# Performance work log

Hardware: AMD Instinct MI355X
Metric: run time of the kernel (lower is better)

Reference implementation:

```python
import jax, jax.numpy as jnp
import numpy as np

LN_EPS = 1e-5


def _layernorm_hd(x, gamma, beta):
    # normalize jointly over the last two dims (H, D), matching nn.LayerNorm((H, D))
    m = jnp.mean(x, axis=(-2, -1), keepdims=True)
    v = jnp.var(x, axis=(-2, -1), keepdims=True)
    return (x - m) * jax.lax.rsqrt(v + LN_EPS) * gamma + beta


def setup_inputs() -> dict:
    B, S, H, D = 4, 4096, 8, 64
    key = jax.random.key(0)
    k1, k2, k3 = jax.random.split(key, 3)
    heads_input = jax.random.normal(k1, (B, S, H, D), dtype=jnp.float32)
    W_hid = jax.random.normal(k2, (2 * D, 3 * D), dtype=jnp.float32) * (1.0 / np.sqrt(2 * D))
    b_hid = jnp.zeros((3 * D,), dtype=jnp.float32)
    W_og = jax.random.normal(k3, (2 * D, D), dtype=jnp.float32) * (1.0 / np.sqrt(2 * D))
    b_og = jnp.zeros((D,), dtype=jnp.float32)
    ln_gamma = jnp.ones((H, D), dtype=jnp.float32)
    ln_beta = jnp.zeros((H, D), dtype=jnp.float32)
    init_cx = jnp.zeros((H, D), dtype=jnp.float32)
    return {"heads_input": heads_input, "W_hid": W_hid, "b_hid": b_hid,
            "W_og": W_og, "b_og": b_og, "ln_gamma": ln_gamma,
            "ln_beta": ln_beta, "init_cx": init_cx}


def reference(heads_input, W_hid, b_hid, W_og, b_og, ln_gamma, ln_beta, init_cx):
    B, S, H, D = heads_input.shape
    # RS1cumsumFunc: exclusive (right-shifted) cumsum along seq of detached input
    x_det = jax.lax.stop_gradient(heads_input)
    cs = jnp.cumsum(x_det, axis=1)
    csum_raw = jnp.concatenate([jnp.zeros_like(cs[:, :1]), cs[:, :-1]], axis=1)
    csum = _layernorm_hd(csum_raw, ln_gamma, ln_beta)

    # trans_hid on concat(heads_input, csum): [B,S,H,2D] -> [B,S,H,3D]
    hid_in = jnp.concatenate([heads_input, csum], axis=-1)
    h3 = jnp.einsum('bshd,de->bshe', hid_in, W_hid) + b_hid
    igate, fgate, hidden = jnp.split(h3, 3, axis=-1)
    fg = jax.nn.sigmoid(fgate)
    igh = jax.nn.sigmoid(igate) * jax.nn.relu(hidden)

    # LGateFunc: cell_t = fg_t * cell_{t-1} + igh_t, cell_{-1} = init_cx
    def combine(c1, c2):
        a1, b1 = c1
        a2, b2 = c2
        return a1 * a2, b1 * a2 + b2

    a, b = jax.lax.associative_scan(combine, (fg, igh), axis=1)
    cell = a * init_cx + b  # init_cx [H,D] broadcasts over [B,S,H,D]

    og_in = jnp.concatenate([heads_input, cell], axis=-1)
    og = jax.nn.sigmoid(jnp.einsum('bshd,de->bshe', og_in, W_og) + b_og)
    return og * cell
```

## Files before the change

kernel.cpp:

```cpp
#include <hip/hip_runtime.h>
#include <math.h>

#define S_   4096
#define H_   8
#define D_   64
#define HD_  512
#define NCH  256
#define LCH  16
#define RC   128

typedef __bf16 bf16x8 __attribute__((ext_vector_type(8)));
typedef float  f32x4  __attribute__((ext_vector_type(4)));

__device__ __forceinline__ float sigm(float v) { return 1.f / (1.f + __expf(-v)); }

__global__ __launch_bounds__(256) void k_wt(const float* __restrict__ Wh,
                                            const float* __restrict__ Wo,
                                            __bf16* __restrict__ WthS,
                                            __bf16* __restrict__ WtoS) {
  int idx = blockIdx.x * 256 + threadIdx.x;
  if (idx < 24576) {
    int k = idx / 192, n = idx % 192;
    int nt = n >> 4, l16 = n & 15;
    int ks = k >> 5, quad = (k >> 3) & 3, j = k & 7;
    WthS[(((ks * 12 + nt) * 64) + quad * 16 + l16) * 8 + j] = (__bf16)Wh[idx];
  } else {
    int j2 = idx - 24576;
    int k = j2 >> 6, n = j2 & 63;
    int nt = n >> 4, l16 = n & 15;
    int ks = k >> 5, quad = (k >> 3) & 3, j = k & 7;
    WtoS[(((ks * 4 + nt) * 64) + quad * 16 + l16) * 8 + j] = (__bf16)Wo[j2];
  }
}

__global__ __launch_bounds__(512) void k_pre(const float* __restrict__ x,
                                             float* __restrict__ sums,
                                             __bf16* __restrict__ Abf) {
  const int t = threadIdx.x, h = t >> 6, d = t & 63;
  const int b = blockIdx.x >> 8, c = blockIdx.x & 255;
  const float* p = x + ((size_t)(b * S_ + c * LCH)) * HD_ + t;
  const size_t rT0 = ((size_t)(b * H_ + h)) * S_ + c * LCH;
  float acc = 0.f;
  #pragma unroll
  for (int i = 0; i < LCH; ++i) {
    float v = p[(size_t)i * HD_];
    acc += v;
    Abf[(rT0 + i) * 128 + d] = (__bf16)v;
  }
  sums[(size_t)blockIdx.x * HD_ + t] = acc;
}

__global__ __launch_bounds__(512) void k_scan_offsets(const float* __restrict__ sums,
                                                      float* __restrict__ offs) {
  const int b = blockIdx.x, t = threadIdx.x;
  float run = 0.f;
  #pragma unroll 16
  for (int c = 0; c < NCH; ++c) {
    size_t idx = ((size_t)b * NCH + c) * HD_ + t;
    float v = sums[idx];
    offs[idx] = run;
    run += v;
  }
}

__global__ __launch_bounds__(512) void k_ln(const float* __restrict__ offs,
                                            const float* __restrict__ gamma,
                                            const float* __restrict__ beta,
                                            __bf16* __restrict__ Abf) {
  __shared__ float2 red[2][8];
  const int t = threadIdx.x, h = t >> 6, d = t & 63;
  const int b = blockIdx.x >> 8, c = blockIdx.x & 255;
  const size_t rT0 = ((size_t)(b * H_ + h)) * S_ + c * LCH;
  float run = offs[(size_t)blockIdx.x * HD_ + t];
  const float g = gamma[t], be = beta[t];
  for (int i = 0; i < LCH; ++i) {
    float xv = (float)Abf[(rT0 + i) * 128 + d];
    float v = run, v2 = run * run;
    #pragma unroll
    for (int o = 32; o; o >>= 1) { v += __shfl_xor(v, o); v2 += __shfl_xor(v2, o); }
    if ((t & 63) == 0) red[i & 1][h] = make_float2(v, v2);
    __syncthreads();
    float s1 = 0.f, s2 = 0.f;
    #pragma unroll
    for (int w = 0; w < 8; ++w) { s1 += red[i & 1][w].x; s2 += red[i & 1][w].y; }
    float m = s1 * (1.f / HD_);
    float var = fmaf(-m, m, s2 * (1.f / HD_));
    float inv = rsqrtf(var + 1e-5f);
    Abf[(rT0 + i) * 128 + 64 + d] = (__bf16)((run - m) * inv * g + be);
    run += xv;
  }
}

__global__ __launch_bounds__(256) void k_gates(const __bf16* __restrict__ Abf,
                                               const __bf16* __restrict__ WthS,
                                               const float* __restrict__ bh,
                                               float* __restrict__ cA,
                                               float* __restrict__ cB) {
  const int t = threadIdx.x;
  const int wave = t >> 6, lane = t & 63;
  const int quad = lane >> 4, l16 = lane & 15;
  const int b = blockIdx.x >> 8, c = blockIdx.x & 255;

  f32x4 acc[2][12];
  #pragma unroll
  for (int i = 0; i < 2; ++i)
    #pragma unroll
    for (int j = 0; j < 12; ++j) acc[i][j] = (f32x4){0.f, 0.f, 0.f, 0.f};

  #pragma unroll
  for (int ks = 0; ks < 4; ++ks) {
    bf16x8 bfrag[12];
    #pragma unroll
    for (int nt = 0; nt < 12; ++nt)
      bfrag[nt] = *(const bf16x8*)(WthS + (size_t)((ks * 12 + nt) * 64 + lane) * 8);
    #pragma unroll
    for (int mi = 0; mi < 2; ++mi) {
      int h = wave * 2 + mi;
      size_t arow = ((size_t)(b * H_ + h)) * S_ + c * LCH + l16;
      bf16x8 afrag = *(const bf16x8*)(Abf + arow * 128 + ks * 32 + quad * 8);
      #pragma unroll
      for (int nt = 0; nt < 12; ++nt)
        acc[mi][nt] = __builtin_amdgcn_mfma_f32_16x16x32_bf16(afrag, bfrag[nt], acc[mi][nt], 0, 0, 0);
    }
  }

  #pragma unroll
  for (int mi = 0; mi < 2; ++mi) {
    int h = wave * 2 + mi;
    #pragma unroll
    for (int nt = 0; nt < 4; ++nt) {
      int d = nt * 16 + l16;
      float bi = bh[d], bf = bh[64 + d], bhv = bh[128 + d];
      float A = 1.f, Bv = 0.f;
      #pragma unroll
      for (int r = 0; r < 4; ++r) {
        float f = sigm(acc[mi][nt + 4][r] + bf);
        float g = sigm(acc[mi][nt][r] + bi) * fmaxf(acc[mi][nt + 8][r] + bhv, 0.f);
        A = f * A;
        Bv = fmaf(f, Bv, g);
      }
      float At = 0.f, Bt = 0.f;
      #pragma unroll
      for (int q = 0; q < 4; ++q) {
        float Aq = __shfl(A, q * 16 + l16);
        float Bq = __shfl(Bv, q * 16 + l16);
        if (q == 0) { At = Aq; Bt = Bq; }
        else { At = Aq * At; Bt = fmaf(Aq, Bt, Bq); }
      }
      if (quad == 0) {
        cA[(size_t)blockIdx.x * HD_ + h * 64 + d] = At;
        cB[(size_t)blockIdx.x * HD_ + h * 64 + d] = Bt;
      }
    }
  }
}

__global__ __launch_bounds__(512) void k_cell_scan(const float* __restrict__ cA,
                                                   const float* __restrict__ cB,
                                                   const float* __restrict__ initcx,
                                                   float* __restrict__ cin) {
  const int b = blockIdx.x, t = threadIdx.x;
  float run = initcx[t];
  #pragma unroll 16
  for (int c = 0; c < NCH; ++c) {
    size_t idx = ((size_t)b * NCH + c) * HD_ + t;
    float a = cA[idx], bb = cB[idx];
    cin[idx] = run;
    run = fmaf(a, run, bb);
  }
}

__global__ __launch_bounds__(256) void k_og(const __bf16* __restrict__ Abf,
                                            const __bf16* __restrict__ WthS,
                                            const float* __restrict__ bh,
                                            const __bf16* __restrict__ WtoS,
                                            const float* __restrict__ bo,
                                            const float* __restrict__ cin,
                                            float* __restrict__ out) {
  __shared__ float cl[RC * 68];
  const int t = threadIdx.x;
  const int wave = t >> 6, lane = t & 63;
  const int quad = lane >> 4, l16 = lane & 15;
  const int b = blockIdx.x >> 8, c = blockIdx.x & 255;

  f32x4 acc[2][12];
  #pragma unroll
  for (int i = 0; i < 2; ++i)
    #pragma unroll
    for (int j = 0; j < 12; ++j) acc[i][j] = (f32x4){0.f, 0.f, 0.f, 0.f};

  #pragma unroll
  for (int ks = 0; ks < 4; ++ks) {
    bf16x8 bfrag[12];
    #pragma unroll
    for (int nt = 0; nt < 12; ++nt)
      bfrag[nt] = *(const bf16x8*)(WthS + (size_t)((ks * 12 + nt) * 64 + lane) * 8);
    #pragma unroll
    for (int mi = 0; mi < 2; ++mi) {
      int h = wave * 2 + mi;
      size_t arow = ((size_t)(b * H_ + h)) * S_ + c * LCH + l16;
      bf16x8 afrag = *(const bf16x8*)(Abf + arow * 128 + ks * 32 + quad * 8);
      #pragma unroll
      for (int nt = 0; nt < 12; ++nt)
        acc[mi][nt] = __builtin_amdgcn_mfma_f32_16x16x32_bf16(afrag, bfrag[nt], acc[mi][nt], 0, 0, 0);
    }
  }

  #pragma unroll
  for (int mi = 0; mi < 2; ++mi) {
    int h = wave * 2 + mi;
    #pragma unroll
    for (int nt = 0; nt < 4; ++nt) {
      int d = nt * 16 + l16;
      float bi = bh[d], bf = bh[64 + d], bhv = bh[128 + d];
      float fr[4], gr[4];
      float A = 1.f, Bv = 0.f;
      #pragma unroll
      for (int r = 0; r < 4; ++r) {
        fr[r] = sigm(acc[mi][nt + 4][r] + bf);
        gr[r] = sigm(acc[mi][nt][r] + bi) * fmaxf(acc[mi][nt + 8][r] + bhv, 0.f);
        A = fr[r] * A;
        Bv = fmaf(fr[r], Bv, gr[r]);
      }
      float cv = cin[(size_t)blockIdx.x * HD_ + h * 64 + d];
      #pragma unroll
      for (int q = 0; q < 3; ++q) {
        float Aq = __shfl(A, q * 16 + l16);
        float Bq = __shfl(Bv, q * 16 + l16);
        if (q < quad) cv = fmaf(Aq, cv, Bq);
      }
      #pragma unroll
      for (int r = 0; r < 4; ++r) {
        cv = fmaf(fr[r], cv, gr[r]);
        cl[(h * 16 + quad * 4 + r) * 68 + d] = cv;
      }
    }
  }

  f32x4 acc2[2][4];
  #pragma unroll
  for (int i = 0; i < 2; ++i)
    #pragma unroll
    for (int j = 0; j < 4; ++j) acc2[i][j] = (f32x4){0.f, 0.f, 0.f, 0.f};

  #pragma unroll
  for (int ks = 0; ks < 4; ++ks) {
    bf16x8 bfrag[4];
    #pragma unroll
    for (int nt = 0; nt < 4; ++nt)
      bfrag[nt] = *(const bf16x8*)(WtoS + (size_t)((ks * 4 + nt) * 64 + lane) * 8);
    #pragma unroll
    for (int mi = 0; mi < 2; ++mi) {
      int h = wave * 2 + mi;
      bf16x8 afrag;
      if (ks < 2) {
        size_t arow = ((size_t)(b * H_ + h)) * S_ + c * LCH + l16;
        afrag = *(const bf16x8*)(Abf + arow * 128 + ks * 32 + quad * 8);
      } else {
        const float* src = &cl[(h * 16 + l16) * 68 + (ks - 2) * 32 + quad * 8];
        #pragma unroll
        for (int j = 0; j < 8; ++j) afrag[j] = (__bf16)src[j];
      }
      #pragma unroll
      for (int nt = 0; nt < 4; ++nt)
        acc2[mi][nt] = __builtin_amdgcn_mfma_f32_16x16x32_bf16(afrag, bfrag[nt], acc2[mi][nt], 0, 0, 0);
    }
  }

  #pragma unroll
  for (int mi = 0; mi < 2; ++mi) {
    int h = wave * 2 + mi;
    #pragma unroll
    for (int nt = 0; nt < 4; ++nt) {
      int d = nt * 16 + l16;
      float bv = bo[d];
      #pragma unroll
      for (int r = 0; r < 4; ++r) {
        int s = quad * 4 + r;
        float og = sigm(acc2[mi][nt][r] + bv);
        cl[(h * 16 + s) * 68 + d] = og * cl[(h * 16 + s) * 68 + d];
      }
    }
  }
  __syncthreads();

  const size_t base4 = (size_t)blockIdx.x * 2048;
  #pragma unroll
  for (int rep = 0; rep < 8; ++rep) {
    int j = rep * 256 + t;
    int s = j >> 7, h2 = (j >> 4) & 7, d4 = j & 15;
    float4 v = *(const float4*)&cl[(h2 * 16 + s) * 68 + d4 * 4];
    ((float4*)out)[base4 + j] = v;
  }
}

extern "C" void kernel_launch(void* const* d_in, const int* in_sizes, int n_in,
                              void* d_out, int out_size, void* d_ws, size_t ws_size,
                              hipStream_t stream) {
  const float* x      = (const float*)d_in[0];
  const float* W_hid  = (const float*)d_in[1];
  const float* b_hid  = (const float*)d_in[2];
  const float* W_og   = (const float*)d_in[3];
  const float* b_og   = (const float*)d_in[4];
  const float* gamma  = (const float*)d_in[5];
  const float* beta   = (const float*)d_in[6];
  const float* initcx = (const float*)d_in[7];
  float* out = (float*)d_out;
  float* ws  = (float*)d_ws;

  const size_t SM = 524288;
  float*  sums = ws;
  float*  offs = sums + SM;
  float*  cA   = offs + SM;
  float*  cB   = cA + SM;
  float*  cin  = cB + SM;
  __bf16* Abf  = (__bf16*)(cin + SM);
  __bf16* WthS = (__bf16*)(Abf + (size_t)131072 * 128);
  __bf16* WtoS = WthS + 24576;

  k_wt          <<<128,  256, 0, stream>>>(W_hid, W_og, WthS, WtoS);
  k_pre         <<<1024, 512, 0, stream>>>(x, sums, Abf);
  k_scan_offsets<<<4,    512, 0, stream>>>(sums, offs);
  k_ln          <<<1024, 512, 0, stream>>>(offs, gamma, beta, Abf);
  k_gates       <<<1024, 256, 0, stream>>>(Abf, WthS, b_hid, cA, cB);
  k_cell_scan   <<<4,    512, 0, stream>>>(cA, cB, initcx, cin);
  k_og          <<<1024, 256, 0, stream>>>(Abf, WthS, b_hid, WtoS, b_og, cin, out);
}
```

Measured before the change: 224.7 us.

## Fuse all stages into one persistent kernel with grid barriers and LDS-resident tiles

Replaces the seven-kernel pipeline with one persistent kernel of 512 blocks that synchronise through an atomic grid barrier. Each block keeps its two chunks' bf16 input and layernormed cumsum tiles in swizzled LDS across all phases, so the global bf16 staging buffer and its round trips go away. The two sequential scans run on 8 blocks between barriers, and the output is written straight from registers rather than staged through LDS. The cost is 64KB of LDS per block, which limits occupancy, plus idle blocks during the scan phases. Correctness depends on all 512 blocks being co-resident, otherwise the barrier deadlocks.

```diff
diff --git a/kernel.cpp b/kernel.cpp
--- a/kernel.cpp
+++ b/kernel.cpp
@@ -3,294 +3,294 @@
 
 #define S_   4096
 #define H_   8
-#define D_   64
 #define HD_  512
 #define NCH  256
 #define LCH  16
-#define RC   128
 
 typedef __bf16 bf16x8 __attribute__((ext_vector_type(8)));
 typedef float  f32x4  __attribute__((ext_vector_type(4)));
 
 __device__ __forceinline__ float sigm(float v) { return 1.f / (1.f + __expf(-v)); }
 
-__global__ __launch_bounds__(256) void k_wt(const float* __restrict__ Wh,
-                                            const float* __restrict__ Wo,
-                                            __bf16* __restrict__ WthS,
-                                            __bf16* __restrict__ WtoS) {
-  int idx = blockIdx.x * 256 + threadIdx.x;
-  if (idx < 24576) {
-    int k = idx / 192, n = idx % 192;
-    int nt = n >> 4, l16 = n & 15;
-    int ks = k >> 5, quad = (k >> 3) & 3, j = k & 7;
-    WthS[(((ks * 12 + nt) * 64) + quad * 16 + l16) * 8 + j] = (__bf16)Wh[idx];
-  } else {
-    int j2 = idx - 24576;
-    int k = j2 >> 6, n = j2 & 63;
-    int nt = n >> 4, l16 = n & 15;
-    int ks = k >> 5, quad = (k >> 3) & 3, j = k & 7;
-    WtoS[(((ks * 4 + nt) * 64) + quad * 16 + l16) * 8 + j] = (__bf16)Wo[j2];
-  }
+__device__ __forceinline__ int swz(int row, int k) {
+  return ((((k >> 3) ^ (row & 15)) << 3) | (k & 7));
 }
 
-__global__ __launch_bounds__(512) void k_pre(const float* __restrict__ x,
-                                             float* __restrict__ sums,
-                                             __bf16* __restrict__ Abf) {
-  const int t = threadIdx.x, h = t >> 6, d = t & 63;
-  const int b = blockIdx.x >> 8, c = blockIdx.x & 255;
-  const float* p = x + ((size_t)(b * S_ + c * LCH)) * HD_ + t;
-  const size_t rT0 = ((size_t)(b * H_ + h)) * S_ + c * LCH;
-  float acc = 0.f;
-  #pragma unroll
-  for (int i = 0; i < LCH; ++i) {
-    float v = p[(size_t)i * HD_];
-    acc += v;
-    Abf[(rT0 + i) * 128 + d] = (__bf16)v;
-  }
-  sums[(size_t)blockIdx.x * HD_ + t] = acc;
+__device__ __forceinline__ void gridbar(int* bar, int target) {
+  __threadfence();
+  __syncthreads();
+  if (threadIdx.x == 0) {
+    __hip_atomic_fetch_add(bar, 1, __ATOMIC_RELEASE, __HIP_MEMORY_SCOPE_AGENT);
+    int v;
+    do {
+      v = __hip_atomic_load(bar, __ATOMIC_ACQUIRE, __HIP_MEMORY_SCOPE_AGENT);
+      if (v < target) __builtin_amdgcn_s_sleep(4);
+    } while (v < target);
+  }
+  __syncthreads();
+  __threadfence();
 }
 
-__global__ __launch_bounds__(512) void k_scan_offsets(const float* __restrict__ sums,
-                                                      float* __restrict__ offs) {
-  const int b = blockIdx.x, t = threadIdx.x;
-  float run = 0.f;
-  #pragma unroll 16
-  for (int c = 0; c < NCH; ++c) {
-    size_t idx = ((size_t)b * NCH + c) * HD_ + t;
-    float v = sums[idx];
-    offs[idx] = run;
-    run += v;
-  }
-}
-
-__global__ __launch_bounds__(512) void k_ln(const float* __restrict__ offs,
-                                            const float* __restrict__ gamma,
-                                            const float* __restrict__ beta,
-                                            __bf16* __restrict__ Abf) {
-  __shared__ float2 red[2][8];
-  const int t = threadIdx.x, h = t >> 6, d = t & 63;
-  const int b = blockIdx.x >> 8, c = blockIdx.x & 255;
-  const size_t rT0 = ((size_t)(b * H_ + h)) * S_ + c * LCH;
-  float run = offs[(size_t)blockIdx.x * HD_ + t];
-  const float g = gamma[t], be = beta[t];
-  for (int i = 0; i < LCH; ++i) {
-    float xv = (float)Abf[(rT0 + i) * 128 + d];
-    float v = run, v2 = run * run;
-    #pragma unroll
-    for (int o = 32; o; o >>= 1) { v += __shfl_xor(v, o); v2 += __shfl_xor(v2, o); }
-    if ((t & 63) == 0) red[i & 1][h] = make_float2(v, v2);
-    __syncthreads();
-    float s1 = 0.f, s2 = 0.f;
-    #pragma unroll
-    for (int w = 0; w < 8; ++w) { s1 += red[i & 1][w].x; s2 += red[i & 1][w].y; }
-    float m = s1 * (1.f / HD_);
-    float var = fmaf(-m, m, s2 * (1.f / HD_));
-    float inv = rsqrtf(var + 1e-5f);
-    Abf[(rT0 + i) * 128 + 64 + d] = (__bf16)((run - m) * inv * g + be);
-    run += xv;
-  }
-}
-
-__global__ __launch_bounds__(256) void k_gates(const __bf16* __restrict__ Abf,
-                                               const __bf16* __restrict__ WthS,
-                                               const float* __restrict__ bh,
-                                               float* __restrict__ cA,
-                                               float* __restrict__ cB) {
-  const int t = threadIdx.x;
+__global__ void k_init(int* bar) { *bar = 0; }
+
+__global__ __launch_bounds__(256, 2) void k_fused(
+    const float* __restrict__ x, const float* __restrict__ Wh,
+    const float* __restrict__ bh, const float* __restrict__ Wo,
+    const float* __restrict__ bo, const float* __restrict__ gamma,
+    const float* __restrict__ beta, const float* __restrict__ initcx,
+    float* __restrict__ out,
+    float* __restrict__ sums, float* __restrict__ offs,
+    float* __restrict__ cA, float* __restrict__ cB, float* __restrict__ cin,
+    __bf16* __restrict__ WthS, __bf16* __restrict__ WtoS, int* bar) {
+  __shared__ __bf16 At[2 * 128 * 128];
+  const int t = threadIdx.x, blk = blockIdx.x;
   const int wave = t >> 6, lane = t & 63;
   const int quad = lane >> 4, l16 = lane & 15;
-  const int b = blockIdx.x >> 8, c = blockIdx.x & 255;
-
-  f32x4 acc[2][12];
+
   #pragma unroll
-  for (int i = 0; i < 2; ++i)
-    #pragma unroll
-    for (int j = 0; j < 12; ++j) acc[i][j] = (f32x4){0.f, 0.f, 0.f, 0.f};
-
+  for (int cc = 0; cc < 2; ++cc) {
+    int g = blk * 2 + cc, b = g >> 8, c = g & 255;
+    int hd0 = t * 2, h = hd0 >> 6, d0 = hd0 & 63;
+    const float2* xp = (const float2*)(x + ((size_t)(b * S_ + c * LCH)) * HD_) + t;
+    float a0 = 0.f, a1 = 0.f;
+    #pragma unroll
+    for (int s = 0; s < LCH; ++s) {
+      float2 v = xp[s * 256];
+      a0 += v.x; a1 += v.y;
+      int row = h * LCH + s;
+      __bf16* base = &At[cc * 16384 + row * 128];
+      base[swz(row, d0)]     = (__bf16)v.x;
+      base[swz(row, d0 + 1)] = (__bf16)v.y;
+    }
+    ((float2*)(sums + (size_t)g * HD_))[t] = make_float2(a0, a1);
+  }
+  if (blk < 128) {
+    int idx = blk * 256 + t;
+    if (idx < 24576) {
+      int k = idx / 192, n = idx % 192;
+      int nt = n >> 4, j16 = n & 15;
+      int ks = k >> 5, q = (k >> 3) & 3, j = k & 7;
+      WthS[(((ks * 12 + nt) * 64) + q * 16 + j16) * 8 + j] = (__bf16)Wh[idx];
+    } else {
+      int j2 = idx - 24576, k = j2 >> 6, n = j2 & 63;
+      int nt = n >> 4, j16 = n & 15;
+      int ks = k >> 5, q = (k >> 3) & 3, j = k & 7;
+      WtoS[(((ks * 4 + nt) * 64) + q * 16 + j16) * 8 + j] = (__bf16)Wo[j2];
+    }
+  }
+  gridbar(bar, 512);
+
+  if (blk < 8) {
+    int batch = blk >> 1, half = blk & 1, hd = half * 256 + t;
+    float run = 0.f;
+    #pragma unroll 8
+    for (int c = 0; c < NCH; ++c) {
+      size_t idx = ((size_t)batch * NCH + c) * HD_ + hd;
+      float v = sums[idx];
+      offs[idx] = run;
+      run += v;
+    }
+  }
+  gridbar(bar, 1024);
+
+  float ga[8], be8[8];
   #pragma unroll
-  for (int ks = 0; ks < 4; ++ks) {
-    bf16x8 bfrag[12];
-    #pragma unroll
-    for (int nt = 0; nt < 12; ++nt)
-      bfrag[nt] = *(const bf16x8*)(WthS + (size_t)((ks * 12 + nt) * 64 + lane) * 8);
+  for (int h = 0; h < 8; ++h) { ga[h] = gamma[h * 64 + lane]; be8[h] = beta[h * 64 + lane]; }
+
+  #pragma unroll 1
+  for (int cc = 0; cc < 2; ++cc) {
+    int g = blk * 2 + cc;
+    {
+      float run[8];
+      #pragma unroll
+      for (int h = 0; h < 8; ++h) run[h] = offs[(size_t)g * HD_ + h * 64 + lane];
+      for (int s = 0; s < LCH; ++s) {
+        float xv[8], p1 = 0.f, p2 = 0.f;
+        #pragma unroll
+        for (int h = 0; h < 8; ++h) {
+          int row = h * 16 + s;
+          xv[h] = (float)At[cc * 16384 + row * 128 + swz(row, lane)];
+          p1 += run[h];
+          p2 += run[h] * run[h];
+        }
+        #pragma unroll
+        for (int o = 32; o; o >>= 1) { p1 += __shfl_xor(p1, o); p2 += __shfl_xor(p2, o); }
+        float m = p1 * (1.f / HD_);
+        float var = fmaf(-m, m, p2 * (1.f / HD_));
+        float inv = rsqrtf(var + 1e-5f);
+        #pragma unroll
+        for (int hh = 0; hh < 2; ++hh) {
+          int h = wave * 2 + hh, row = h * 16 + s;
+          At[cc * 16384 + row * 128 + swz(row, 64 + lane)] =
+              (__bf16)((run[h] - m) * inv * ga[h] + be8[h]);
+        }
+        #pragma unroll
+        for (int h = 0; h < 8; ++h) run[h] += xv[h];
+      }
+    }
+    __syncthreads();
+
+    f32x4 acc[2][12];
+    #pragma unroll
+    for (int i = 0; i < 2; ++i)
+      #pragma unroll
+      for (int j = 0; j < 12; ++j) acc[i][j] = (f32x4){0.f, 0.f, 0.f, 0.f};
+    #pragma unroll
+    for (int ks = 0; ks < 4; ++ks) {
+      bf16x8 bfrag[12];
+      #pragma unroll
+      for (int nt = 0; nt < 12; ++nt)
+        bfrag[nt] = *(const bf16x8*)(WthS + (size_t)((ks * 12 + nt) * 64 + lane) * 8);
+      #pragma unroll
+      for (int mi = 0; mi < 2; ++mi) {
+        int h = wave * 2 + mi, row = h * 16 + l16;
+        int pg = (ks * 4 + quad) ^ (row & 15);
+        bf16x8 afrag = *(const bf16x8*)&At[cc * 16384 + row * 128 + pg * 8];
+        #pragma unroll
+        for (int nt = 0; nt < 12; ++nt)
+          acc[mi][nt] = __builtin_amdgcn_mfma_f32_16x16x32_bf16(afrag, bfrag[nt], acc[mi][nt], 0, 0, 0);
+      }
+    }
     #pragma unroll
     for (int mi = 0; mi < 2; ++mi) {
       int h = wave * 2 + mi;
-      size_t arow = ((size_t)(b * H_ + h)) * S_ + c * LCH + l16;
-      bf16x8 afrag = *(const bf16x8*)(Abf + arow * 128 + ks * 32 + quad * 8);
+      #pragma unroll
+      for (int nt = 0; nt < 4; ++nt) {
+        int d = nt * 16 + l16;
+        float bi = bh[d], bf = bh[64 + d], bhv = bh[128 + d];
+        float A = 1.f, Bv = 0.f;
+        #pragma unroll
+        for (int r = 0; r < 4; ++r) {
+          float f = sigm(acc[mi][nt + 4][r] + bf);
+          float gg = sigm(acc[mi][nt][r] + bi) * fmaxf(acc[mi][nt + 8][r] + bhv, 0.f);
+          A = f * A;
+          Bv = fmaf(f, Bv, gg);
+        }
+        float Atot = 0.f, Btot = 0.f;
+        #pragma unroll
+        for (int q = 0; q < 4; ++q) {
+          float Aq = __shfl(A, q * 16 + l16);
+          float Bq = __shfl(Bv, q * 16 + l16);
+          if (q == 0) { Atot = Aq; Btot = Bq; }
+          else { Atot = Aq * Atot; Btot = fmaf(Aq, Btot, Bq); }
+        }
+        if (quad == 0) {
+          cA[(size_t)g * HD_ + h * 64 + d] = Atot;
+          cB[(size_t)g * HD_ + h * 64 + d] = Btot;
+        }
+      }
+    }
+    __syncthreads();
+  }
+  gridbar(bar, 1536);
+
+  if (blk < 8) {
+    int batch = blk >> 1, half = blk & 1, hd = half * 256 + t;
+    float run = initcx[hd];
+    #pragma unroll 8
+    for (int c = 0; c < NCH; ++c) {
+      size_t idx = ((size_t)batch * NCH + c) * HD_ + hd;
+      float a = cA[idx], bb = cB[idx];
+      cin[idx] = run;
+      run = fmaf(a, run, bb);
+    }
+  }
+  gridbar(bar, 2048);
+
+  #pragma unroll 1
+  for (int cc = 0; cc < 2; ++cc) {
+    int g = blk * 2 + cc, b = g >> 8, c = g & 255;
+    f32x4 acc[2][12];
+    #pragma unroll
+    for (int i = 0; i < 2; ++i)
+      #pragma unroll
+      for (int j = 0; j < 12; ++j) acc[i][j] = (f32x4){0.f, 0.f, 0.f, 0.f};
+    #pragma unroll
+    for (int ks = 0; ks < 4; ++ks) {
+      bf16x8 bfrag[12];
       #pragma unroll
       for (int nt = 0; nt < 12; ++nt)
-        acc[mi][nt] = __builtin_amdgcn_mfma_f32_16x16x32_bf16(afrag, bfrag[nt], acc[mi][nt], 0, 0, 0);
-    }
-  }
-
-  #pragma unroll
-  for (int mi = 0; mi < 2; ++mi) {
-    int h = wave * 2 + mi;
-    #pragma unroll
-    for (int nt = 0; nt < 4; ++nt) {
-      int d = nt * 16 + l16;
-      float bi = bh[d], bf = bh[64 + d], bhv = bh[128 + d];
-      float A = 1.f, Bv = 0.f;
-      #pragma unroll
-      for (int r = 0; r < 4; ++r) {
-        float f = sigm(acc[mi][nt + 4][r] + bf);
-        float g = sigm(acc[mi][nt][r] + bi) * fmaxf(acc[mi][nt + 8][r] + bhv, 0.f);
-        A = f * A;
-        Bv = fmaf(f, Bv, g);
-      }
-      float At = 0.f, Bt = 0.f;
-      #pragma unroll
-      for (int q = 0; q < 4; ++q) {
-        float Aq = __shfl(A, q * 16 + l16);
-        float Bq = __shfl(Bv, q * 16 + l16);
-        if (q == 0) { At = Aq; Bt = Bq; }
-        else { At = Aq * At; Bt = fmaf(Aq, Bt, Bq); }
-      }
-      if (quad == 0) {
-        cA[(size_t)blockIdx.x * HD_ + h * 64 + d] = At;
-        cB[(size_t)blockIdx.x * HD_ + h * 64 + d] = Bt;
-      }
-    }
-  }
-}
-
-__global__ __launch_bounds__(512) void k_cell_scan(const float* __restrict__ cA,
-                                                   const float* __restrict__ cB,
-                                                   const float* __restrict__ initcx,
-                                                   float* __restrict__ cin) {
-  const int b = blockIdx.x, t = threadIdx.x;
-  float run = initcx[t];
-  #pragma unroll 16
-  for (int c = 0; c < NCH; ++c) {
-    size_t idx = ((size_t)b * NCH + c) * HD_ + t;
-    float a = cA[idx], bb = cB[idx];
-    cin[idx] = run;
-    run = fmaf(a, run, bb);
-  }
-}
-
-__global__ __launch_bounds__(256) void k_og(const __bf16* __restrict__ Abf,
-                                            const __bf16* __restrict__ WthS,
-                                            const float* __restrict__ bh,
-                                            const __bf16* __restrict__ WtoS,
-                                            const float* __restrict__ bo,
-                                            const float* __restrict__ cin,
-                                            float* __restrict__ out) {
-  __shared__ float cl[RC * 68];
-  const int t = threadIdx.x;
-  const int wave = t >> 6, lane = t & 63;
-  const int quad = lane >> 4, l16 = lane & 15;
-  const int b = blockIdx.x >> 8, c = blockIdx.x & 255;
-
-  f32x4 acc[2][12];
-  #pragma unroll
-  for (int i = 0; i < 2; ++i)
-    #pragma unroll
-    for (int j = 0; j < 12; ++j) acc[i][j] = (f32x4){0.f, 0.f, 0.f, 0.f};
-
-  #pragma unroll
-  for (int ks = 0; ks < 4; ++ks) {
-    bf16x8 bfrag[12];
-    #pragma unroll
-    for (int nt = 0; nt < 12; ++nt)
-      bfrag[nt] = *(const bf16x8*)(WthS + (size_t)((ks * 12 + nt) * 64 + lane) * 8);
+        bfrag[nt] = *(const bf16x8*)(WthS + (size_t)((ks * 12 + nt) * 64 + lane) * 8);
+      #pragma unroll
+      for (int mi = 0; mi < 2; ++mi) {
+        int h = wave * 2 + mi, row = h * 16 + l16;
+        int pg = (ks * 4 + quad) ^ (row & 15);
+        bf16x8 afrag = *(const bf16x8*)&At[cc * 16384 + row * 128 + pg * 8];
+        #pragma unroll
+        for (int nt = 0; nt < 12; ++nt)
+          acc[mi][nt] = __builtin_amdgcn_mfma_f32_16x16x32_bf16(afrag, bfrag[nt], acc[mi][nt], 0, 0, 0);
+      }
+    }
+    float cellreg[2][4][4];
     #pragma unroll
     for (int mi = 0; mi < 2; ++mi) {
       int h = wave * 2 + mi;
-      size_t arow = ((size_t)(b * H_ + h)) * S_ + c * LCH + l16;
-      bf16x8 afrag = *(const bf16x8*)(Abf + arow * 128 + ks * 32 + quad * 8);
-      #pragma unroll
-      for (int nt = 0; nt < 12; ++nt)
-        acc[mi][nt] = __builtin_amdgcn_mfma_f32_16x16x32_bf16(afrag, bfrag[nt], acc[mi][nt], 0, 0, 0);
-    }
-  }
-
-  #pragma unroll
-  for (int mi = 0; mi < 2; ++mi) {
-    int h = wave * 2 + mi;
-    #pragma unroll
-    for (int nt = 0; nt < 4; ++nt) {
-      int d = nt * 16 + l16;
-      float bi = bh[d], bf = bh[64 + d], bhv = bh[128 + d];
-      float fr[4], gr[4];
-      float A = 1.f, Bv = 0.f;
-      #pragma unroll
-      for (int r = 0; r < 4; ++r) {
-        fr[r] = sigm(acc[mi][nt + 4][r] + bf);
-        gr[r] = sigm(acc[mi][nt][r] + bi) * fmaxf(acc[mi][nt + 8][r] + bhv, 0.f);
-        A = fr[r] * A;
-        Bv = fmaf(fr[r], Bv, gr[r]);
-      }
-      float cv = cin[(size_t)blockIdx.x * HD_ + h * 64 + d];
-      #pragma unroll
-      for (int q = 0; q < 3; ++q) {
-        float Aq = __shfl(A, q * 16 + l16);
-        float Bq = __shfl(Bv, q * 16 + l16);
-        if (q < quad) cv = fmaf(Aq, cv, Bq);
-      }
-      #pragma unroll
-      for (int r = 0; r < 4; ++r) {
-        cv = fmaf(fr[r], cv, gr[r]);
-        cl[(h * 16 + quad * 4 + r) * 68 + d] = cv;
-      }
-    }
-  }
-
-  f32x4 acc2[2][4];
-  #pragma unroll
-  for (int i = 0; i < 2; ++i)
-    #pragma unroll
-    for (int j = 0; j < 4; ++j) acc2[i][j] = (f32x4){0.f, 0.f, 0.f, 0.f};
-
-  #pragma unroll
-  for (int ks = 0; ks < 4; ++ks) {
-    bf16x8 bfrag[4];
-    #pragma unroll
-    for (int nt = 0; nt < 4; ++nt)
-      bfrag[nt] = *(const bf16x8*)(WtoS + (size_t)((ks * 4 + nt) * 64 + lane) * 8);
+      #pragma unroll
+      for (int nt = 0; nt < 4; ++nt) {
+        int d = nt * 16 + l16;
+        float bi = bh[d], bf = bh[64 + d], bhv = bh[128 + d];
+        float fr[4], gr[4];
+        float A = 1.f, Bv = 0.f;
+        #pragma unroll
+        for (int r = 0; r < 4; ++r) {
+          fr[r] = sigm(acc[mi][nt + 4][r] + bf);
+          gr[r] = sigm(acc[mi][nt][r] + bi) * fmaxf(acc[mi][nt + 8][r] + bhv, 0.f);
+          A = fr[r] * A;
+          Bv = fmaf(fr[r], Bv, gr[r]);
+        }
+        float cv = cin[(size_t)g * HD_ + h * 64 + d];
+        #pragma unroll
+        for (int q = 0; q < 3; ++q) {
+          float Aq = __shfl(A, q * 16 + l16);
+          float Bq = __shfl(Bv, q * 16 + l16);
+          if (q < quad) cv = fmaf(Aq, cv, Bq);
+        }
+        #pragma unroll
+        for (int r = 0; r < 4; ++r) {
+          cv = fmaf(fr[r], cv, gr[r]);
+          cellreg[mi][nt][r] = cv;
+          int row = h * 16 + quad * 4 + r;
+          At[cc * 16384 + row * 128 + swz(row, 64 + d)] = (__bf16)cv;
+        }
+      }
+    }
+    f32x4 acc2[2][4];
+    #pragma unroll
+    for (int i = 0; i < 2; ++i)
+      #pragma unroll
+      for (int j = 0; j < 4; ++j) acc2[i][j] = (f32x4){0.f, 0.f, 0.f, 0.f};
+    #pragma unroll
+    for (int ks = 0; ks < 4; ++ks) {
+      bf16x8 bfrag[4];
+      #pragma unroll
+      for (int nt = 0; nt < 4; ++nt)
+        bfrag[nt] = *(const bf16x8*)(WtoS + (size_t)((ks * 4 + nt) * 64 + lane) * 8);
+      #pragma unroll
+      for (int mi = 0; mi < 2; ++mi) {
+        int h = wave * 2 + mi, row = h * 16 + l16;
+        int pg = (ks * 4 + quad) ^ (row & 15);
+        bf16x8 afrag = *(const bf16x8*)&At[cc * 16384 + row * 128 + pg * 8];
+        #pragma unroll
+        for (int nt = 0; nt < 4; ++nt)
+          acc2[mi][nt] = __builtin_amdgcn_mfma_f32_16x16x32_bf16(afrag, bfrag[nt], acc2[mi][nt], 0, 0, 0);
+      }
+    }
     #pragma unroll
     for (int mi = 0; mi < 2; ++mi) {
       int h = wave * 2 + mi;
-      bf16x8 afrag;
-      if (ks < 2) {
-        size_t arow = ((size_t)(b * H_ + h)) * S_ + c * LCH + l16;
-        afrag = *(const bf16x8*)(Abf + arow * 128 + ks * 32 + quad * 8);
-      } else {
-        const float* src = &cl[(h * 16 + l16) * 68 + (ks - 2) * 32 + quad * 8];
-        #pragma unroll
-        for (int j = 0; j < 8; ++j) afrag[j] = (__bf16)src[j];
-      }
-      #pragma unroll
-      for (int nt = 0; nt < 4; ++nt)
-        acc2[mi][nt] = __builtin_amdgcn_mfma_f32_16x16x32_bf16(afrag, bfrag[nt], acc2[mi][nt], 0, 0, 0);
-    }
-  }
-
-  #pragma unroll
-  for (int mi = 0; mi < 2; ++mi) {
-    int h = wave * 2 + mi;
-    #pragma unroll
-    for (int nt = 0; nt < 4; ++nt) {
-      int d = nt * 16 + l16;
-      float bv = bo[d];
-      #pragma unroll
-      for (int r = 0; r < 4; ++r) {
-        int s = quad * 4 + r;
-        float og = sigm(acc2[mi][nt][r] + bv);
-        cl[(h * 16 + s) * 68 + d] = og * cl[(h * 16 + s) * 68 + d];
-      }
-    }
-  }
-  __syncthreads();
-
-  const size_t base4 = (size_t)blockIdx.x * 2048;
-  #pragma unroll
-  for (int rep = 0; rep < 8; ++rep) {
-    int j = rep * 256 + t;
-    int s = j >> 7, h2 = (j >> 4) & 7, d4 = j & 15;
-    float4 v = *(const float4*)&cl[(h2 * 16 + s) * 68 + d4 * 4];
-    ((float4*)out)[base4 + j] = v;
+      #pragma unroll
+      for (int nt = 0; nt < 4; ++nt) {
+        int d = nt * 16 + l16;
+        float bv = bo[d];
+        #pragma unroll
+        for (int r = 0; r < 4; ++r) {
+          int s = quad * 4 + r;
+          float og = sigm(acc2[mi][nt][r] + bv);
+          out[((size_t)((b * S_ + c * LCH + s) * H_ + h)) * 64 + d] = og * cellreg[mi][nt][r];
+        }
+      }
+    }
+    __syncthreads();
   }
 }
 
@@ -309,20 +309,17 @@
   float* ws  = (float*)d_ws;
 
   const size_t SM = 524288;
-  float*  sums = ws;
+  int*    bar  = (int*)ws;
+  float*  sums = ws + 16;
   float*  offs = sums + SM;
-  float*  cA   = offs + SM;
-  float*  cB   = cA + SM;
-  float*  cin  = cB + SM;
-  __bf16* Abf  = (__bf16*)(cin + SM);
-  __bf16* WthS = (__bf16*)(Abf + (size_t)131072 * 128);
+  float*  cAp  = offs + SM;
+  float*  cBp  = cAp + SM;
+  float*  cinp = cBp + SM;
+  __bf16* WthS = (__bf16*)(cinp + SM);
   __bf16* WtoS = WthS + 24576;
 
-  k_wt          <<<128,  256, 0, stream>>>(W_hid, W_og, WthS, WtoS);
-  k_pre         <<<1024, 512, 0, stream>>>(x, sums, Abf);
-  k_scan_offsets<<<4,    512, 0, stream>>>(sums, offs);
-  k_ln          <<<1024, 512, 0, stream>>>(offs, gamma, beta, Abf);
-  k_gates       <<<1024, 256, 0, stream>>>(Abf, WthS, b_hid, cA, cB);
-  k_cell_scan   <<<4,    512, 0, stream>>>(cA, cB, initcx, cin);
-  k_og          <<<1024, 256, 0, stream>>>(Abf, WthS, b_hid, WtoS, b_og, cin, out);
+  k_init<<<1, 1, 0, stream>>>(bar);
+  k_fused<<<512, 256, 0, stream>>>(x, W_hid, b_hid, W_og, b_og, gamma, beta,
+                                   initcx, out, sums, offs, cAp, cBp, cinp,
+                                   WthS, WtoS, bar);
 }
```

Result: slower. 820.9 us (+265.4%).
